# Kernel optimization log

Measured on AMD Instinct MI355X. Metric: run time of the kernel, lower is better.

Reference implementation:

```python
import jax, jax.numpy as jnp
import numpy as np

SIZE_IN = 1024
SIZE_OUT = 1024
N_ROWS = 16384
MAX_VAL = 127.0  # nemo=False -> int8 path


def _quantize(t, max_val):
    """Per-tensor symmetric quantization matching the torch code.
    scale = max_val / max(|min(t)|, |max(t)|) (1.0 if t_max==0);
    q = clamp(round(scale*t), -max_val, max_val) cast to int8."""
    t_max = jnp.maximum(jnp.abs(jnp.min(t)), jnp.abs(jnp.max(t)))
    t_max = jnp.where(t_max == 0.0, 1.0, t_max)
    scale = max_val / t_max
    q = jnp.clip(jnp.round(scale * t), -max_val, max_val).astype(jnp.int8)
    return q, scale


def setup_inputs() -> dict:
    key = jax.random.key(0)
    kx, kw, kb = jax.random.split(key, 3)
    x = jax.random.normal(kx, (N_ROWS, SIZE_IN), dtype=jnp.float32)
    # kaiming_uniform_(a=sqrt(5)) -> uniform(-1/sqrt(fan_in), 1/sqrt(fan_in))
    bound = 1.0 / np.sqrt(SIZE_IN)
    weight = jax.random.uniform(kw, (SIZE_OUT, SIZE_IN), dtype=jnp.float32,
                                minval=-bound, maxval=bound)
    bias = jax.random.uniform(kb, (SIZE_OUT,), dtype=jnp.float32,
                              minval=-bound, maxval=bound)
    return {"x": x, "weight": weight, "bias": bias}


def reference(x, weight, bias):
    qw, sw = _quantize(weight, MAX_VAL)          # [SIZE_OUT, SIZE_IN] int8
    qx, sa = _quantize(x, MAX_VAL)               # [N, SIZE_IN] int8
    qb, sb = _quantize(bias, MAX_VAL)            # [SIZE_OUT] int8
    # for the approximate axx kernel), then dequantize.
    acc = jnp.matmul(qx.astype(jnp.int32), qw.astype(jnp.int32).T)  # [N, SIZE_OUT]
    out = acc.astype(jnp.float32) / (sa * sw)
    out = out + qb.astype(jnp.float32) / sb
    return out
```

## Files before the change

kernel.cpp:

```cpp
#include <hip/hip_runtime.h>


#define M_ROWS 16384
#define K_DIM  1024
#define N_OUT  1024

typedef int v4i __attribute__((ext_vector_type(4)));

__device__ __forceinline__ void gload_lds16(const void* g, void* l) {
  __builtin_amdgcn_global_load_lds(
      (const __attribute__((address_space(1))) void*)g,
      (__attribute__((address_space(3))) void*)l, 16, 0, 0);
}

__device__ __forceinline__ float block_reduce_max4(float m, float* red) {
#pragma unroll
  for (int off = 32; off > 0; off >>= 1)
    m = fmaxf(m, __shfl_down(m, off));
  const int wid = threadIdx.x >> 6, lane = threadIdx.x & 63;
  if (lane == 0) red[wid] = m;
  __syncthreads();
  float r = fmaxf(fmaxf(red[0], red[1]), fmaxf(red[2], red[3]));
  __syncthreads();
  return r;
}

__global__ void amax_stage1(const float* __restrict__ src, int n4,
                            float* __restrict__ partials) {
  __shared__ float red[4];
  float m = 0.0f;
  const int stride = gridDim.x * blockDim.x;
  for (int idx = blockIdx.x * blockDim.x + threadIdx.x; idx < n4; idx += stride) {
    float4 v = ((const float4*)src)[idx];
    m = fmaxf(m, fmaxf(fmaxf(fabsf(v.x), fabsf(v.y)), fmaxf(fabsf(v.z), fabsf(v.w))));
  }
  float r = block_reduce_max4(m, red);
  if (threadIdx.x == 0) partials[blockIdx.x] = r;
}

__global__ void finalize_kernel(const float* __restrict__ px, int npx,
                                const float* __restrict__ pw, int npw,
                                const float* __restrict__ bias,
                                float* __restrict__ amax,
                                float* __restrict__ bdeq) {
  __shared__ float red[4];
  const int tid = threadIdx.x;

  float m = 0.0f;
  for (int i = tid; i < npx; i += 256) m = fmaxf(m, px[i]);
  float rx = block_reduce_max4(m, red);

  m = 0.0f;
  for (int i = tid; i < npw; i += 256) m = fmaxf(m, pw[i]);
  float rw = block_reduce_max4(m, red);

  float4 bv = ((const float4*)bias)[tid];
  m = fmaxf(fmaxf(fabsf(bv.x), fabsf(bv.y)), fmaxf(fabsf(bv.z), fabsf(bv.w)));
  float rb = block_reduce_max4(m, red);

  if (rx == 0.0f) rx = 1.0f;
  if (rw == 0.0f) rw = 1.0f;
  if (rb == 0.0f) rb = 1.0f;
  if (tid == 0) {
    amax[0] = rx;
    amax[1] = rw;
    amax[2] = rb;
  }
  const float sb = 127.0f / rb;
  float4 q;
  q.x = fminf(fmaxf(rintf(sb * bv.x), -127.0f), 127.0f) / sb;
  q.y = fminf(fmaxf(rintf(sb * bv.y), -127.0f), 127.0f) / sb;
  q.z = fminf(fmaxf(rintf(sb * bv.z), -127.0f), 127.0f) / sb;
  q.w = fminf(fmaxf(rintf(sb * bv.w), -127.0f), 127.0f) / sb;
  ((float4*)bdeq)[tid] = q;
}

__global__ void quant_kernel(const float* __restrict__ src, signed char* __restrict__ dst,
                             int n4, const float* __restrict__ amax, int slot) {
  const float s = 127.0f / amax[slot];
  const int stride = gridDim.x * blockDim.x;
  for (int idx = blockIdx.x * blockDim.x + threadIdx.x; idx < n4; idx += stride) {
    float4 v = ((const float4*)src)[idx];
    int q0 = (int)fminf(fmaxf(rintf(s * v.x), -127.0f), 127.0f);
    int q1 = (int)fminf(fmaxf(rintf(s * v.y), -127.0f), 127.0f);
    int q2 = (int)fminf(fmaxf(rintf(s * v.z), -127.0f), 127.0f);
    int q3 = (int)fminf(fmaxf(rintf(s * v.w), -127.0f), 127.0f);
    unsigned int packed = (q0 & 0xff) | ((q1 & 0xff) << 8) |
                          ((q2 & 0xff) << 16) | ((q3 & 0xff) << 24);
    ((unsigned int*)dst)[idx] = packed;
  }
}


__global__ __launch_bounds__(512, 2) void gemm_kernel(
    const signed char* __restrict__ qx, const signed char* __restrict__ qw,
    const float* __restrict__ amax, const float* __restrict__ bdeq,
    float* __restrict__ out) {
  __shared__ char lds[131072];

  const int tid  = threadIdx.x;
  const int w    = tid >> 6;
  const int lane = tid & 63;
  const int wm = w >> 2;
  const int wn = w & 3;
  const int fr = lane & 15;
  const int q  = lane >> 4;

  const int bid = blockIdx.x;
  const int wg  = (bid & 7) * 32 + (bid >> 3);
  const int Mbase = (wg >> 2) * 256;
  const int Nbase = (wg & 3) * 256;

  const signed char* gA = qx + (size_t)Mbase * K_DIM;
  const signed char* gB = qw + (size_t)Nbase * K_DIM;

  const int lrow = lane >> 3;
  const int lcol = ((lane & 7) ^ lrow) << 4;

  const int u0    = (q ^ (fr & 7)) << 4;
  const int aoffA = (wm * 64 + fr) * 128 + u0;
  const int aoffB = (wn * 32 + fr) * 128 + u0;

  v4i acc[8][4] = {};

#define STG(MAT, BUF, HALF, T)                                                 \
  do {                                                                         \
    const signed char* _gb = (MAT) ? gB : gA;                                  \
    char* _l = lds + ((MAT) ? 65536 : 0) + (BUF)*32768 + (HALF)*16384 +        \
               w * 2048;                                                       \
    size_t _ro = (size_t)((HALF)*128 + w * 16 + lrow) * K_DIM + (T)*128 + lcol;\
    gload_lds16(_gb + _ro, _l);                                                \
    gload_lds16(_gb + _ro + (size_t)8 * K_DIM, _l + 1024);                     \
  } while (0)

#define PHASE(BUF, MH, NH, STAGE_STMT, VM4)                                    \
  do {                                                                         \
    const char* _A = lds + (BUF)*32768 + (MH)*16384;                           \
    const char* _B = lds + 65536 + (BUF)*32768 + (NH)*16384;                   \
    v4i _a[4][2], _b[2][2];                                                    \
    _Pragma("unroll") for (int f = 0; f < 4; ++f) {                            \
      _a[f][0] = *(const v4i*)(_A + (aoffA + f * 2048));                       \
      _a[f][1] = *(const v4i*)(_A + ((aoffA ^ 64) + f * 2048));                \
    }                                                                          \
    _Pragma("unroll") for (int g = 0; g < 2; ++g) {                            \
      _b[g][0] = *(const v4i*)(_B + (aoffB + g * 2048));                       \
      _b[g][1] = *(const v4i*)(_B + ((aoffB ^ 64) + g * 2048));                \
    }                                                                          \
    STAGE_STMT;                                                                \
    __builtin_amdgcn_s_barrier();                                              \
    asm volatile("s_waitcnt lgkmcnt(0)" ::: "memory");                         \
    __builtin_amdgcn_sched_barrier(0);                                         \
    __builtin_amdgcn_s_setprio(1);                                             \
    _Pragma("unroll") for (int kk = 0; kk < 2; ++kk)                           \
      _Pragma("unroll") for (int f = 0; f < 4; ++f)                            \
        _Pragma("unroll") for (int g = 0; g < 2; ++g)                          \
          acc[(MH)*4 + f][(NH)*2 + g] = __builtin_amdgcn_mfma_i32_16x16x64_i8( \
              _a[f][kk], _b[g][kk], acc[(MH)*4 + f][(NH)*2 + g], 0, 0, 0);     \
    __builtin_amdgcn_s_setprio(0);                                             \
    if (VM4) { asm volatile("s_waitcnt vmcnt(4)" ::: "memory"); }              \
    __builtin_amdgcn_s_barrier();                                              \
  } while (0)

  STG(0, 0, 0, 0); STG(1, 0, 0, 0);
  STG(0, 0, 1, 0); STG(1, 0, 1, 0);
  STG(0, 1, 0, 1); STG(1, 1, 0, 1);
  asm volatile("s_waitcnt vmcnt(4)" ::: "memory");
  __builtin_amdgcn_s_barrier();

  for (int j = 0; j < 4; ++j) {
    const int t1 = 2 * j + 1;
    const int t2 = (2 * j + 2) & 7;
    const int t3 = (2 * j + 3) & 7;
    PHASE(0, 0, 0, STG(0, 1, 1, t1), 0);
    PHASE(0, 0, 1, STG(1, 1, 1, t1), 0);
    PHASE(0, 1, 0, STG(0, 0, 0, t2), 0);
    PHASE(0, 1, 1, STG(1, 0, 0, t2), 1);
    PHASE(1, 0, 0, STG(0, 0, 1, t2), 0);
    PHASE(1, 0, 1, STG(1, 0, 1, t2), 0);
    PHASE(1, 1, 0, STG(0, 1, 0, t3), 0);
    PHASE(1, 1, 1, STG(1, 1, 0, t3), 1);
  }
#undef PHASE
#undef STG

  const float inv_denom = (amax[0] * amax[1]) * (1.0f / 16129.0f);
#pragma unroll
  for (int f = 0; f < 8; ++f) {
    const int row0 = Mbase + wm * 64 + (f & 3) * 16 + (f >> 2) * 128 + q * 4;
#pragma unroll
    for (int g = 0; g < 4; ++g) {
      const int col = Nbase + wn * 32 + (g & 1) * 16 + (g >> 1) * 128 + fr;
      const float bb = bdeq[col];
#pragma unroll
      for (int i = 0; i < 4; ++i) {
        out[(size_t)(row0 + i) * N_OUT + col] = (float)acc[f][g][i] * inv_denom + bb;
      }
    }
  }
}

extern "C" void kernel_launch(void* const* d_in, const int* in_sizes, int n_in,
                              void* d_out, int out_size, void* d_ws, size_t ws_size,
                              hipStream_t stream) {
  const float* x = (const float*)d_in[0];
  const float* w = (const float*)d_in[1];
  const float* b = (const float*)d_in[2];
  float* out = (float*)d_out;

  char* ws = (char*)d_ws;
  float* amax = (float*)ws;
  float* bdeq = (float*)(ws + 256);
  float* px   = (float*)(ws + 8192);
  float* pw   = (float*)(ws + 16384 + 8192);
  signed char* qw = (signed char*)(ws + 65536);
  signed char* qx = (signed char*)(ws + (1 << 21));

  const int NPX = 2048, NPW = 256;
  hipLaunchKernelGGL(amax_stage1, dim3(NPX), dim3(256), 0, stream, x, M_ROWS * K_DIM / 4, px);
  hipLaunchKernelGGL(amax_stage1, dim3(NPW), dim3(256), 0, stream, w, N_OUT * K_DIM / 4, pw);
  hipLaunchKernelGGL(finalize_kernel, dim3(1), dim3(256), 0, stream, px, NPX, pw, NPW, b, amax, bdeq);
  hipLaunchKernelGGL(quant_kernel, dim3(2048), dim3(256), 0, stream, x, qx, M_ROWS * K_DIM / 4, amax, 0);
  hipLaunchKernelGGL(quant_kernel, dim3(256), dim3(256), 0, stream, w, qw, N_OUT * K_DIM / 4, amax, 1);
  hipLaunchKernelGGL(gemm_kernel, dim3(64 * 4), dim3(512), 0, stream, qx, qw, amax, bdeq, out);
}
```

Measured before the change: 68.34 us.

## Reuse A/B fragments in registers across quadrant MFMA phases and deepen prefetch

Restructures the GEMM main loop so A and B LDS fragments are held in registers and reused across quadrant phases, using a snake order (00,01,11,10). This cuts LDS reads per K-tile from four A+B pairs to about two of each. The prologue now stages both halves of the second buffer up front, and global->LDS stages are rescheduled with adjusted vmcnt waits. It raises register pressure for the extra B buffers and makes the buffer hazard/wait ordering more delicate.

```diff
diff --git a/kernel.cpp b/kernel.cpp
--- a/kernel.cpp
+++ b/kernel.cpp
@@ -122,6 +122,8 @@
   const int aoffB = (wn * 32 + fr) * 128 + u0;
 
   v4i acc[8][4] = {};
+  v4i Ar[4][2];
+  v4i Br[2][2][2];
 
 #define STG(MAT, BUF, HALF, T)                                                 \
   do {                                                                         \
@@ -133,20 +135,26 @@
     gload_lds16(_gb + _ro + (size_t)8 * K_DIM, _l + 1024);                     \
   } while (0)
 
-#define PHASE(BUF, MH, NH, STAGE_STMT, VM4)                                    \
+#define RD_A(BUF, MH)                                                          \
   do {                                                                         \
     const char* _A = lds + (BUF)*32768 + (MH)*16384;                           \
+    _Pragma("unroll") for (int f = 0; f < 4; ++f) {                            \
+      Ar[f][0] = *(const v4i*)(_A + (aoffA + f * 2048));                       \
+      Ar[f][1] = *(const v4i*)(_A + ((aoffA ^ 64) + f * 2048));                \
+    }                                                                          \
+  } while (0)
+
+#define RD_B(BUF, NH)                                                          \
+  do {                                                                         \
     const char* _B = lds + 65536 + (BUF)*32768 + (NH)*16384;                   \
-    v4i _a[4][2], _b[2][2];                                                    \
-    _Pragma("unroll") for (int f = 0; f < 4; ++f) {                            \
-      _a[f][0] = *(const v4i*)(_A + (aoffA + f * 2048));                       \
-      _a[f][1] = *(const v4i*)(_A + ((aoffA ^ 64) + f * 2048));                \
+    _Pragma("unroll") for (int g = 0; g < 2; ++g) {                            \
+      Br[NH][g][0] = *(const v4i*)(_B + (aoffB + g * 2048));                   \
+      Br[NH][g][1] = *(const v4i*)(_B + ((aoffB ^ 64) + g * 2048));            \
     }                                                                          \
-    _Pragma("unroll") for (int g = 0; g < 2; ++g) {                            \
-      _b[g][0] = *(const v4i*)(_B + (aoffB + g * 2048));                       \
-      _b[g][1] = *(const v4i*)(_B + ((aoffB ^ 64) + g * 2048));                \
-    }                                                                          \
-    STAGE_STMT;                                                                \
+  } while (0)
+
+#define MM(MH, NH)                                                             \
+  do {                                                                         \
     __builtin_amdgcn_s_barrier();                                              \
     asm volatile("s_waitcnt lgkmcnt(0)" ::: "memory");                         \
     __builtin_amdgcn_sched_barrier(0);                                         \
@@ -155,33 +163,36 @@
       _Pragma("unroll") for (int f = 0; f < 4; ++f)                            \
         _Pragma("unroll") for (int g = 0; g < 2; ++g)                          \
           acc[(MH)*4 + f][(NH)*2 + g] = __builtin_amdgcn_mfma_i32_16x16x64_i8( \
-              _a[f][kk], _b[g][kk], acc[(MH)*4 + f][(NH)*2 + g], 0, 0, 0);     \
+              Ar[f][kk], Br[NH][g][kk], acc[(MH)*4 + f][(NH)*2 + g], 0, 0, 0); \
     __builtin_amdgcn_s_setprio(0);                                             \
-    if (VM4) { asm volatile("s_waitcnt vmcnt(4)" ::: "memory"); }              \
-    __builtin_amdgcn_s_barrier();                                              \
-  } while (0)
-
-  STG(0, 0, 0, 0); STG(1, 0, 0, 0);
-  STG(0, 0, 1, 0); STG(1, 0, 1, 0);
-  STG(0, 1, 0, 1); STG(1, 1, 0, 1);
-  asm volatile("s_waitcnt vmcnt(4)" ::: "memory");
-  __builtin_amdgcn_s_barrier();
+  } while (0)
+
+#define VM(N) asm volatile("s_waitcnt vmcnt(" #N ")" ::: "memory")
+#define BAR() __builtin_amdgcn_s_barrier()
+
+  STG(0, 0, 0, 0); STG(1, 0, 0, 0); STG(1, 0, 1, 0); STG(0, 0, 1, 0);
+  STG(0, 1, 0, 1); STG(1, 1, 0, 1); STG(1, 1, 1, 1); STG(0, 1, 1, 1);
+  VM(8);
+  BAR();
 
   for (int j = 0; j < 4; ++j) {
-    const int t1 = 2 * j + 1;
     const int t2 = (2 * j + 2) & 7;
     const int t3 = (2 * j + 3) & 7;
-    PHASE(0, 0, 0, STG(0, 1, 1, t1), 0);
-    PHASE(0, 0, 1, STG(1, 1, 1, t1), 0);
-    PHASE(0, 1, 0, STG(0, 0, 0, t2), 0);
-    PHASE(0, 1, 1, STG(1, 0, 0, t2), 1);
-    PHASE(1, 0, 0, STG(0, 0, 1, t2), 0);
-    PHASE(1, 0, 1, STG(1, 0, 1, t2), 0);
-    PHASE(1, 1, 0, STG(0, 1, 0, t3), 0);
-    PHASE(1, 1, 1, STG(1, 1, 0, t3), 1);
-  }
-#undef PHASE
+    RD_A(0, 0); RD_B(0, 0);                    MM(0, 0);        BAR();
+    RD_B(0, 1); STG(0, 0, 0, t2);              MM(0, 1);        BAR();
+    RD_A(0, 1); STG(1, 0, 0, t2);              MM(1, 1);        BAR();
+    STG(1, 0, 1, t2);                          MM(1, 0); VM(6); BAR();
+    RD_A(1, 0); RD_B(1, 0); STG(0, 0, 1, t2);  MM(0, 0);        BAR();
+    RD_B(1, 1); STG(0, 1, 0, t3); STG(1, 1, 0, t3); MM(0, 1);   BAR();
+    RD_A(1, 1); STG(1, 1, 1, t3);              MM(1, 1);        BAR();
+    STG(0, 1, 1, t3);                          MM(1, 0); VM(8); BAR();
+  }
+#undef MM
+#undef RD_A
+#undef RD_B
 #undef STG
+#undef VM
+#undef BAR
 
   const float inv_denom = (amax[0] * amax[1]) * (1.0f / 16129.0f);
 #pragma unroll
```

Result: faster. 65.62 us (-4.0%).
